# Performance work log

Hardware: AMD Instinct MI355X
Metric: run time of the kernel (lower is better)

## Reference

```python
import jax, jax.numpy as jnp
import numpy as np
from jax import lax

B, N, C, H = 16, 577, 1024, 16
D = C // H          # head_dim = 64
M = 24              # spatial side, M*M = N-1
CH = C // 4         # conv bottleneck channels = 256
EPS = 1e-5


def _ln(x, g, b):
    mu = jnp.mean(x, axis=-1, keepdims=True)
    var = jnp.mean((x - mu) ** 2, axis=-1, keepdims=True)
    return (x - mu) * lax.rsqrt(var + EPS) * g + b


def setup_inputs() -> dict:
    key = jax.random.key(0)
    ks = jax.random.split(key, 8)
    s = 0.02
    return {
        "x": jax.random.normal(ks[0], (B, N, C), jnp.float32),
        "ln1_g": jnp.ones((C,), jnp.float32),
        "ln1_b": jnp.zeros((C,), jnp.float32),
        "in_w": jax.random.normal(ks[1], (3 * C, C), jnp.float32) * s,
        "in_b": jnp.zeros((3 * C,), jnp.float32),
        "out_w": jax.random.normal(ks[2], (C, C), jnp.float32) * s,
        "out_b": jnp.zeros((C,), jnp.float32),
        "ln2_g": jnp.ones((C,), jnp.float32),
        "ln2_b": jnp.zeros((C,), jnp.float32),
        "conv1_w": jax.random.normal(ks[3], (CH, C, 3, 3), jnp.float32) * s,
        "conv1_b": jnp.zeros((CH,), jnp.float32),
        "conv2_w": jax.random.normal(ks[4], (C, CH, 3, 3), jnp.float32) * s,
        "conv2_b": jnp.zeros((C,), jnp.float32),
    }


def reference(x, ln1_g, ln1_b, in_w, in_b, out_w, out_b, ln2_g, ln2_b,
              conv1_w, conv1_b, conv2_w, conv2_b):
    residual = x
    h = _ln(x, ln1_g, ln1_b)
    # qkv projection: (B,N,3C) -> (3,B,H,N,D)
    qkv = (h @ in_w.T + in_b).reshape(B, N, 3, H, D).transpose(2, 0, 3, 1, 4)
    q, k, v = qkv[0], qkv[1], qkv[2]
    scale = D ** (-0.5)
    scores = jnp.einsum("bhnd,bhmd->bhnm", q, k) * scale   # (B,H,N,N)
    attn = jax.nn.softmax(scores, axis=-1)
    o = jnp.einsum("bhnm,bhmd->bhnd", attn, v)
    o = o.transpose(0, 2, 1, 3).reshape(B, N, C)
    o = o @ out_w.T + out_b
    x = o + residual                                       # first residual

    y = _ln(x, ln2_g, ln2_b)
    f = y[:, :-1, :].reshape(B, M, M, C).transpose(0, 3, 1, 2)   # NCHW
    c = y[:, -1:, :]                                             # class token
    f = lax.conv_general_dilated(f, conv1_w, (1, 1), "SAME",
                                 dimension_numbers=("NCHW", "OIHW", "NCHW"))
    f = jax.nn.gelu(f + conv1_b[None, :, None, None])
    f = lax.conv_general_dilated(f, conv2_w, (1, 1), "SAME",
                                 dimension_numbers=("NCHW", "OIHW", "NCHW"))
    f = f + conv2_b[None, :, None, None]
    f = f.transpose(0, 2, 3, 1).reshape(B, N - 1, C)
    y = jnp.concatenate((f, c), axis=1)
    return x + y
```

## Files before the change

### kernel.cpp

```cpp
#include <hip/hip_runtime.h>

typedef unsigned short u16;
typedef unsigned int u32;
typedef __bf16 bf16x8 __attribute__((ext_vector_type(8)));
typedef float f32x4 __attribute__((ext_vector_type(4)));

#define DEVI __device__ __forceinline__

#define BB 16
#define NN 577
#define CC 1024
#define HH 16
#define DD 64
#define BN 9232
#define PIX 576
#define WW 24
#define CHN 256
#define VROW 584
#define PSZ (9216 * 256)

DEVI u16 f2b(float f) {
  u32 u = __builtin_bit_cast(u32, f);
  u32 r = 0x7FFFu + ((u >> 16) & 1u);
  return (u16)((u + r) >> 16);
}

DEVI float b2f(u16 h) { return __builtin_bit_cast(float, (u32)h << 16); }

DEVI bf16x8 ldfrag(const u16* p) {
  uint4 u = *(const uint4*)p;
  return __builtin_bit_cast(bf16x8, u);
}

DEVI f32x4 mfma16(bf16x8 a, bf16x8 b, f32x4 c) {
  return __builtin_amdgcn_mfma_f32_16x16x32_bf16(a, b, c, 0, 0, 0);
}

DEVI void gld_lds16(const u16* g, u16* l) {
  __builtin_amdgcn_global_load_lds((const __attribute__((address_space(1))) void*)g,
                                   (__attribute__((address_space(3))) void*)l, 16, 0, 0);
}

DEVI float gelu_tanh(float v) {
  const float x3 = v * v * v;
  const float t = __expf(1.5957691216057308f * (v + 0.044715f * x3));
  const float th = (t - 1.f) / (t + 1.f);
  return 0.5f * v * (1.f + th);
}

__global__ __launch_bounds__(256) void prep_kernel(
    const float* __restrict__ in_w, const float* __restrict__ out_w,
    const float* __restrict__ c1w, const float* __restrict__ c2w,
    u16* __restrict__ wqkv, u16* __restrict__ wout,
    u16* __restrict__ w1t, u16* __restrict__ w2t, u16* __restrict__ zpad) {
  const int i0 = blockIdx.x * 256 + threadIdx.x;
  const int stride = gridDim.x * 256;
  for (int i = i0; i < 3072 * 1024; i += stride) wqkv[i] = f2b(in_w[i]);
  for (int i = i0; i < 1024 * 1024; i += stride) wout[i] = f2b(out_w[i]);
  for (int i = i0; i < 256 * 9216; i += stride) {
    int oc = i / 9216, rem = i - oc * 9216, tap = rem >> 10, c = rem & 1023;
    w1t[i] = f2b(c1w[(size_t)oc * 9216 + c * 9 + tap]);
  }
  for (int i = i0; i < 1024 * 2304; i += stride) {
    int oc = i / 2304, rem = i - oc * 2304, tap = rem >> 8, c = rem & 255;
    w2t[i] = f2b(c2w[(size_t)oc * 2304 + c * 9 + tap]);
  }
  if (i0 < 128) zpad[i0] = 0;
}

template <int MODE>
__global__ __launch_bounds__(256) void ln_kernel(
    const float* __restrict__ xin, const float* __restrict__ gam,
    const float* __restrict__ bet, u16* __restrict__ yout, float* __restrict__ oextra) {
  __shared__ float sh[8];
  const int row = blockIdx.x;
  const int tid = threadIdx.x;
  const float4 v = ((const float4*)(xin + (size_t)row * CC))[tid];
  float s = v.x + v.y + v.z + v.w;
  float qq = v.x * v.x + v.y * v.y + v.z * v.z + v.w * v.w;
#pragma unroll
  for (int off = 32; off > 0; off >>= 1) {
    s += __shfl_down(s, off);
    qq += __shfl_down(qq, off);
  }
  if ((tid & 63) == 0) { sh[tid >> 6] = s; sh[4 + (tid >> 6)] = qq; }
  __syncthreads();
  s = sh[0] + sh[1] + sh[2] + sh[3];
  qq = sh[4] + sh[5] + sh[6] + sh[7];
  const float mu = s * (1.f / 1024.f);
  const float rstd = rsqrtf(qq * (1.f / 1024.f) - mu * mu + 1e-5f);
  const float4 g4 = ((const float4*)gam)[tid];
  const float4 b4 = ((const float4*)bet)[tid];
  const float o0 = (v.x - mu) * rstd * g4.x + b4.x;
  const float o1 = (v.y - mu) * rstd * g4.y + b4.y;
  const float o2 = (v.z - mu) * rstd * g4.z + b4.z;
  const float o3 = (v.w - mu) * rstd * g4.w + b4.w;
  ushort4 st = make_ushort4(f2b(o0), f2b(o1), f2b(o2), f2b(o3));
  *(ushort4*)(yout + (size_t)row * CC + tid * 4) = st;
  if constexpr (MODE == 1) {
    if (row % NN == NN - 1) {
      float4 ov = make_float4(v.x + o0, v.y + o1, v.z + o2, v.w + o3);
      ((float4*)(oextra + (size_t)row * CC))[tid] = ov;
    }
  }
}

struct GArgs {
  const u16* A; const u16* Bm; const float* bias; const float* res;
  float* outF; u16* outH; u16* outQ; u16* outK; u16* outV; const u16* zpad;
  int M, K;
};

template <int MODE>
__global__ __launch_bounds__(256) void gemm_kernel(GArgs ag) {
  __shared__ u16 SH[24576];
  const int tid = threadIdx.x;
  const int w = tid >> 6, l = tid & 63;
  const int wr = w >> 1, wc = w & 1;
  const int lr = l & 15, lg = l >> 4;
  const int m0 = blockIdx.x * 128, n0 = blockIdx.y * 128;
  const int tapz = (MODE == 4) ? blockIdx.z : 0;
  const int rA = w * 16 + (l >> 2);
  const int cbs = ((l & 3) ^ ((l >> 3) & 3)) * 8;

  auto stage = [&](int buf, int kt) {
    const int k0 = kt * 32;
    u16* Ald = SH + buf * 4096;
    u16* Bld = SH + 12288 + buf * 4096;
#pragma unroll
    for (int c = 0; c < 2; ++c) {
      const int r = c * 64 + rA;
      const u16* asrc;
      if constexpr (MODE <= 1) {
        int m = m0 + r;
        m = m < ag.M ? m : ag.M - 1;
        asrc = ag.A + (size_t)m * ag.K + (k0 + cbs);
      } else {
        const int m = m0 + r;
        const int b = m / PIX, p = m - b * PIX;
        const int py = p / WW, px = p - py * WW;
        constexpr int CKc = (MODE == 3) ? 256 : 1024;
        const int tap = (MODE == 4) ? tapz : (k0 / CKc);
        const int c0 = (MODE == 4) ? k0 : (k0 - tap * CKc);
        const int py2 = py + (tap / 3) - 1, px2 = px + (tap % 3) - 1;
        if ((u32)py2 < (u32)WW && (u32)px2 < (u32)WW) {
          if constexpr (MODE == 4)
            asrc = ag.A + ((size_t)(b * NN + py2 * WW + px2) * CC + c0 + cbs);
          else
            asrc = ag.A + ((size_t)(b * PIX + py2 * WW + px2) * CHN + c0 + cbs);
        } else {
          asrc = ag.zpad + cbs;
        }
      }
      gld_lds16(asrc, &Ald[c * 2048 + w * 512]);
      const u16* bsrc;
      if constexpr (MODE == 4)
        bsrc = ag.Bm + (size_t)(n0 + r) * 9216 + (tapz * 1024 + k0 + cbs);
      else
        bsrc = ag.Bm + (size_t)(n0 + r) * ag.K + (k0 + cbs);
      gld_lds16(bsrc, &Bld[c * 2048 + w * 512]);
    }
  };

  f32x4 acc[4][4] = {};
  const int KL = (MODE == 4) ? 1024 : ag.K;
  const int nst = KL >> 5;

  stage(0, 0);
  stage(1, 1);

  const int swz = (lr >> 1) & 3;
  int b0 = 0, b1 = 1, b2 = 2;
  for (int kt = 0; kt < nst; ++kt) {
    if (kt + 1 < nst) { asm volatile("s_waitcnt vmcnt(4)" ::: "memory"); }
    else              { asm volatile("s_waitcnt vmcnt(0)" ::: "memory"); }
    __builtin_amdgcn_s_barrier();
    if (kt + 2 < nst) stage(b2, kt + 2);
    bf16x8 af[4], bfr[4];
#pragma unroll
    for (int i = 0; i < 4; ++i)
      af[i] = ldfrag(&SH[b0 * 4096 + (wr * 64 + i * 16 + lr) * 32 + ((lg ^ swz) * 8)]);
#pragma unroll
    for (int i = 0; i < 4; ++i)
      bfr[i] = ldfrag(&SH[12288 + b0 * 4096 + (wc * 64 + i * 16 + lr) * 32 + ((lg ^ swz) * 8)]);
    __builtin_amdgcn_s_setprio(1);
#pragma unroll
    for (int mi = 0; mi < 4; ++mi)
#pragma unroll
      for (int ni = 0; ni < 4; ++ni) acc[mi][ni] = mfma16(af[mi], bfr[ni], acc[mi][ni]);
    __builtin_amdgcn_s_setprio(0);
    const int tmp = b0; b0 = b1; b1 = b2; b2 = tmp;
  }

  if constexpr (MODE == 0) {
    if (n0 >= 2048) {
      __syncthreads();
      const int G0 = m0 + wr * 64;
      const int b0q = G0 / NN;
      const bool ok = (G0 + 63 < ag.M) && (b0q == (G0 + 63) / NN);
      const int h = (n0 + wc * 64 - 2048) >> 6;
      u16* scr = SH + w * 5120;
      if (ok) {
#pragma unroll
        for (int mi = 0; mi < 4; ++mi) {
#pragma unroll
          for (int ni = 0; ni < 4; ++ni) {
            ushort4 st;
            const float bv = ag.bias[n0 + wc * 64 + ni * 16 + lr];
            st.x = f2b(acc[mi][ni][0] + bv);
            st.y = f2b(acc[mi][ni][1] + bv);
            st.z = f2b(acc[mi][ni][2] + bv);
            st.w = f2b(acc[mi][ni][3] + bv);
            *(ushort4*)(scr + (ni * 16 + lr) * 80 + mi * 16 + lg * 4) = st;
          }
        }
        asm volatile("s_waitcnt lgkmcnt(0)" ::: "memory");
        const int nb = G0 - b0q * NN;
        u16* vb = ag.outV + (size_t)((b0q * 16 + h) * 64) * VROW;
#pragma unroll
        for (int pass = 0; pass < 8; ++pass) {
          const int d_ = pass * 8 + (l >> 3);
          const int nn = (l & 7) * 8;
          uint4 vv = *(const uint4*)(scr + d_ * 80 + nn);
          u16* dst = vb + (size_t)d_ * VROW + nb + nn;
          if (!(nb & 1)) {
            ((u32*)dst)[0] = vv.x; ((u32*)dst)[1] = vv.y;
            ((u32*)dst)[2] = vv.z; ((u32*)dst)[3] = vv.w;
          } else {
            u16 tmp[8];
            *(uint4*)tmp = vv;
#pragma unroll
            for (int j = 0; j < 8; ++j) dst[j] = tmp[j];
          }
        }
      } else {
#pragma unroll
        for (int mi = 0; mi < 4; ++mi) {
#pragma unroll
          for (int r = 0; r < 4; ++r) {
            const int row = G0 + mi * 16 + lg * 4 + r;
            if (row >= ag.M) continue;
            const int b = row / NN, n = row - b * NN;
#pragma unroll
            for (int ni = 0; ni < 4; ++ni) {
              const int col = n0 + wc * 64 + ni * 16 + lr;
              const int d = col & 63;
              const float v = acc[mi][ni][r] + ag.bias[col];
              ag.outV[((size_t)((b * 16 + h) * 64 + d)) * VROW + n] = f2b(v);
            }
          }
        }
      }
      return;
    }
#pragma unroll
    for (int mi = 0; mi < 4; ++mi) {
#pragma unroll
      for (int r = 0; r < 4; ++r) {
        const int row = m0 + wr * 64 + mi * 16 + lg * 4 + r;
        if (row >= ag.M) continue;
        const int b = row / NN, n = row - b * NN;
#pragma unroll
        for (int ni = 0; ni < 4; ++ni) {
          const int col = n0 + wc * 64 + ni * 16 + lr;
          const int which = col >> 10, hd = col & 1023, h = hd >> 6, d = hd & 63;
          const float v = acc[mi][ni][r] + ag.bias[col];
          if (which == 0)
            ag.outQ[((size_t)(b * 16 + h) * NN + n) * DD + d] = f2b(v * 0.18033688011112042f);
          else
            ag.outK[((size_t)(b * 16 + h) * NN + n) * DD + d] = f2b(v);
        }
      }
    }
  } else {
#pragma unroll
    for (int mi = 0; mi < 4; ++mi) {
#pragma unroll
      for (int r = 0; r < 4; ++r) {
        const int row = m0 + wr * 64 + mi * 16 + lg * 4 + r;
        if (row >= ag.M) continue;
#pragma unroll
        for (int ni = 0; ni < 4; ++ni) {
          const int col = n0 + wc * 64 + ni * 16 + lr;
          if constexpr (MODE == 4) {
            u16* pb = (tapz < 5) ? ag.outH : ag.outQ;
            const int tl = (tapz < 5) ? tapz : tapz - 5;
            pb[(size_t)tl * PSZ + (size_t)row * CHN + col] = f2b(acc[mi][ni][r]);
          } else {
            const float v = acc[mi][ni][r] + ag.bias[col];
            if constexpr (MODE == 1) {
              const size_t idx = (size_t)row * CC + col;
              ag.outF[idx] = v + ag.res[idx];
            } else {
              const int b = row / PIX, p = row - b * PIX;
              const size_t idx = (size_t)(b * NN + p) * CC + col;
              ag.outF[idx] = v + ag.res[idx];
            }
          }
        }
      }
    }
  }
}

__global__ __launch_bounds__(256) void gelu_reduce_kernel(
    const u16* __restrict__ pA, const u16* __restrict__ pB,
    const float* __restrict__ bias, u16* __restrict__ f1) {
  const size_t i4 = ((size_t)blockIdx.x * 256 + threadIdx.x) * 4;
  const int col = (int)(i4 & 255);
  float s0 = 0.f, s1 = 0.f, s2 = 0.f, s3 = 0.f;
#pragma unroll
  for (int t = 0; t < 5; ++t) {
    ushort4 u = *(const ushort4*)(pA + (size_t)t * PSZ + i4);
    s0 += b2f(u.x); s1 += b2f(u.y); s2 += b2f(u.z); s3 += b2f(u.w);
  }
#pragma unroll
  for (int t = 0; t < 4; ++t) {
    ushort4 u = *(const ushort4*)(pB + (size_t)t * PSZ + i4);
    s0 += b2f(u.x); s1 += b2f(u.y); s2 += b2f(u.z); s3 += b2f(u.w);
  }
  const float4 b4 = *(const float4*)(bias + col);
  ushort4 st = make_ushort4(f2b(gelu_tanh(s0 + b4.x)), f2b(gelu_tanh(s1 + b4.y)),
                            f2b(gelu_tanh(s2 + b4.z)), f2b(gelu_tanh(s3 + b4.w)));
  *(ushort4*)(f1 + i4) = st;
}

__global__ __launch_bounds__(512) void attn_kernel(
    const u16* __restrict__ q, const u16* __restrict__ k,
    const u16* __restrict__ vt, u16* __restrict__ o) {
  __shared__ u16 SH2[24576];
  const int tid = threadIdx.x;
  const int w = tid >> 6, l = tid & 63;
  const int lr = l & 15, lg = l >> 4;
  const int lg4 = lg * 4;
  const int bid = blockIdx.x;
  const int xcd = bid & 7, gg = bid >> 3;
  const int bh = (gg / 5) * 8 + xcd;
  const int qt = gg % 5;
  const int b = bh >> 4, h = bh & 15;

  const u16* qp = q + (size_t)bh * NN * DD;
  const u16* kp = k + (size_t)bh * NN * DD;
  const u16* vp = vt + (size_t)bh * DD * VROW;

  const int qrow = qt * 128 + w * 16 + lr;
  const int qrc = qrow < NN ? qrow : NN - 1;
  const bf16x8 qf0 = ldfrag(qp + (size_t)qrc * DD + lg * 8);
  const bf16x8 qf1 = ldfrag(qp + (size_t)qrc * DD + 32 + lg * 8);

  const int srow = l >> 3;
  const int schk = (l & 7) ^ (srow & 7);
  auto stage = [&](int buf, int kt) {
    const int kb = kt * 64;
    gld_lds16(kp + (size_t)(kb + w * 8 + srow) * DD + schk * 8,
              &SH2[buf * 4096 + w * 512]);
    gld_lds16(vp + (size_t)(w * 8 + srow) * VROW + kb + schk * 8,
              &SH2[8192 + buf * 4096 + w * 512]);
  };

  f32x4 oa[4] = {};
  float mrow = -1e30f;
  float lsum = 0.f;
  u16* pw = &SH2[16384 + w * 1024];
  const int x7 = lr & 7;
  const int x3 = lr & 3;

  stage(0, 0);
  stage(1, 1);

  for (int kt = 0; kt < 10; ++kt) {
    if (kt <= 7) { asm volatile("s_waitcnt vmcnt(2)" ::: "memory"); }
    else         { asm volatile("s_waitcnt vmcnt(0)" ::: "memory"); }
    __builtin_amdgcn_s_barrier();
    const u16* KB = &SH2[(kt & 1) * 4096];
    const u16* VB = &SH2[8192 + (kt & 1) * 4096];
    const int kb = kt * 64;

    f32x4 s[4] = {};
#pragma unroll
    for (int g = 0; g < 4; ++g) {
      const int row = g * 16 + lr;
      const bf16x8 a0 = ldfrag(&KB[row * 64 + ((lg ^ x7) * 8)]);
      const bf16x8 a1 = ldfrag(&KB[row * 64 + (((4 + lg) ^ x7) * 8)]);
      s[g] = mfma16(a0, qf0, s[g]);
      s[g] = mfma16(a1, qf1, s[g]);
    }
    float t[16];
    const bool last = (kt == 9);
#pragma unroll
    for (int g = 0; g < 4; ++g)
#pragma unroll
      for (int r = 0; r < 4; ++r) {
        const int key = kb + g * 16 + lg4 + r;
        t[g * 4 + r] = (!last || key < NN) ? s[g][r] : -3e38f;
      }
    float pmax = t[0];
#pragma unroll
    for (int i = 1; i < 16; ++i) pmax = fmaxf(pmax, t[i]);
    pmax = fmaxf(pmax, __shfl_xor(pmax, 16));
    pmax = fmaxf(pmax, __shfl_xor(pmax, 32));
    if (!__all(pmax <= mrow + 8.f)) {
      const float mn = fmaxf(mrow, pmax);
      const float corr = exp2f(mrow - mn);
      mrow = mn;
      lsum *= corr;
      float bc[4];
#pragma unroll
      for (int r = 0; r < 4; ++r) bc[r] = __shfl(corr, (l & 48) | (lg4 + r));
#pragma unroll
      for (int g = 0; g < 4; ++g)
#pragma unroll
        for (int r = 0; r < 4; ++r) oa[g][r] *= bc[r];
    }
    float ps[16];
    float rsum = 0.f;
#pragma unroll
    for (int i = 0; i < 16; ++i) { ps[i] = exp2f(t[i] - mrow); rsum += ps[i]; }
    rsum += __shfl_xor(rsum, 16);
    rsum += __shfl_xor(rsum, 32);
    lsum += rsum;
#pragma unroll
    for (int g = 0; g < 4; ++g) {
      u32 w0, w1;
      asm("v_cvt_pk_bf16_f32 %0, %1, %2" : "=v"(w0) : "v"(ps[g * 4 + 0]), "v"(ps[g * 4 + 1]));
      asm("v_cvt_pk_bf16_f32 %0, %1, %2" : "=v"(w1) : "v"(ps[g * 4 + 2]), "v"(ps[g * 4 + 3]));
      const int lc = (g & 1) * 2 + (lg >> 1);
      const int off = (g >> 1) * 512 + lr * 32 + ((lc ^ x3) * 8) + (lg & 1) * 4;
      *(uint2*)(&pw[off]) = make_uint2(w0, w1);
    }
    asm volatile("s_waitcnt lgkmcnt(0)" ::: "memory");
    const bf16x8 paf = ldfrag(&pw[lr * 32 + ((lg ^ x3) * 8)]);
    const bf16x8 pbf = ldfrag(&pw[512 + lr * 32 + ((lg ^ x3) * 8)]);
#pragma unroll
    for (int dg = 0; dg < 4; ++dg) {
      const int row = dg * 16 + lr;
      const bf16x8 v0 = ldfrag(&VB[row * 64 + ((lg ^ x7) * 8)]);
      const bf16x8 v1 = ldfrag(&VB[row * 64 + (((4 + lg) ^ x7) * 8)]);
      oa[dg] = mfma16(paf, v0, oa[dg]);
      oa[dg] = mfma16(pbf, v1, oa[dg]);
    }
    asm volatile("s_waitcnt lgkmcnt(0)" ::: "memory");
    __builtin_amdgcn_s_barrier();
    if (kt + 2 <= 9) stage(kt & 1, kt + 2);
  }

  const int nq = qt * 128 + w * 16 + lg4;
  float linv[4];
#pragma unroll
  for (int r = 0; r < 4; ++r) linv[r] = __shfl(lsum, (l & 48) | (lg4 + r));
#pragma unroll
  for (int r = 0; r < 4; ++r) {
    const int n = nq + r;
    if (n >= NN) continue;
    const float inv = 1.0f / linv[r];
#pragma unroll
    for (int g = 0; g < 4; ++g)
      o[(size_t)(b * NN + n) * CC + h * DD + g * 16 + lr] = f2b(oa[g][r] * inv);
  }
}

extern "C" void kernel_launch(void* const* d_in, const int* in_sizes, int n_in,
                              void* d_out, int out_size, void* d_ws, size_t ws_size,
                              hipStream_t stream) {
  const float* x     = (const float*)d_in[0];
  const float* ln1_g = (const float*)d_in[1];
  const float* ln1_b = (const float*)d_in[2];
  const float* in_w  = (const float*)d_in[3];
  const float* in_b  = (const float*)d_in[4];
  const float* out_w = (const float*)d_in[5];
  const float* out_b = (const float*)d_in[6];
  const float* ln2_g = (const float*)d_in[7];
  const float* ln2_b = (const float*)d_in[8];
  const float* c1w   = (const float*)d_in[9];
  const float* c1b   = (const float*)d_in[10];
  const float* c2w   = (const float*)d_in[11];
  const float* c2b   = (const float*)d_in[12];
  float* out = (float*)d_out;

  char* ws = (char*)d_ws;
  size_t off = 0;
  auto alloc = [&](size_t bytes) {
    void* p = ws + off;
    off += (bytes + 255) & ~(size_t)255;
    return p;
  };
  u16* hb   = (u16*)alloc((size_t)BN * CC * 2);
  u16* wqkv = (u16*)alloc((size_t)3072 * 1024 * 2);
  u16* wout = (u16*)alloc((size_t)1024 * 1024 * 2);
  u16* w1t  = (u16*)alloc((size_t)256 * 9216 * 2);
  u16* w2t  = (u16*)alloc((size_t)1024 * 2304 * 2);
  u16* qb   = (u16*)alloc((size_t)256 * NN * DD * 2);
  u16* kb   = (u16*)alloc((size_t)256 * NN * DD * 2);
  u16* vtb  = (u16*)alloc((size_t)256 * DD * VROW * 2 + 16384);
  float* x2 = (float*)alloc((size_t)BN * CC * 4);
  u16* zpad = (u16*)alloc(256);
  u16* ob = hb;
  u16* yb = qb;
  u16* f1 = kb;
  u16* pA = hb;
  u16* pB = vtb;

  prep_kernel<<<1024, 256, 0, stream>>>(in_w, out_w, c1w, c2w, wqkv, wout, w1t, w2t, zpad);
  ln_kernel<0><<<BN, 256, 0, stream>>>(x, ln1_g, ln1_b, hb, nullptr);
  {
    GArgs a{hb, wqkv, in_b, nullptr, nullptr, nullptr, qb, kb, vtb, zpad, BN, CC};
    gemm_kernel<0><<<dim3(73, 24), 256, 0, stream>>>(a);
  }
  attn_kernel<<<1280, 512, 0, stream>>>(qb, kb, vtb, ob);
  {
    GArgs a{ob, wout, out_b, x, x2, nullptr, nullptr, nullptr, nullptr, zpad, BN, CC};
    gemm_kernel<1><<<dim3(73, 8), 256, 0, stream>>>(a);
  }
  ln_kernel<1><<<BN, 256, 0, stream>>>(x2, ln2_g, ln2_b, yb, out);
  {
    GArgs a{yb, w1t, c1b, nullptr, nullptr, pA, pB, nullptr, nullptr, zpad, 9216, 9216};
    gemm_kernel<4><<<dim3(72, 2, 9), 256, 0, stream>>>(a);
  }
  gelu_reduce_kernel<<<2304, 256, 0, stream>>>(pA, pB, c1b, f1);
  {
    GArgs a{f1, w2t, c2b, x2, out, nullptr, nullptr, nullptr, nullptr, zpad, 9216, 2304};
    gemm_kernel<3><<<dim3(72, 8), 256, 0, stream>>>(a);
  }
}
```

Before: 399.4 us.

## Enlarge GEMM tiles to 256x128, remap block order, store residual x2 in bf16

The GEMM kernel now computes 256x128 output tiles, with each wave holding 8x4 MFMA accumulators. It uses a 1-D grid with a custom block-to-tile mapping so that neighbouring blocks share weight or activation tiles, and it sets launch bounds to two blocks per CU. The intermediate residual x2 is stored as bf16 instead of fp32, halving that tensor's write and read traffic in the out-proj epilogue, LN2 and the conv2 epilogue. The larger tiles raise register and LDS use and may lower occupancy. The bf16 residual loses precision in the final sum.

```diff
diff --git a/kernel.cpp b/kernel.cpp
--- a/kernel.cpp
+++ b/kernel.cpp
@@ -70,12 +70,19 @@
 
 template <int MODE>
 __global__ __launch_bounds__(256) void ln_kernel(
-    const float* __restrict__ xin, const float* __restrict__ gam,
-    const float* __restrict__ bet, u16* __restrict__ yout, float* __restrict__ oextra) {
+    const float* __restrict__ xf, const u16* __restrict__ xh,
+    const float* __restrict__ gam, const float* __restrict__ bet,
+    u16* __restrict__ yout, float* __restrict__ oextra) {
   __shared__ float sh[8];
   const int row = blockIdx.x;
   const int tid = threadIdx.x;
-  const float4 v = ((const float4*)(xin + (size_t)row * CC))[tid];
+  float4 v;
+  if constexpr (MODE == 0) {
+    v = ((const float4*)(xf + (size_t)row * CC))[tid];
+  } else {
+    ushort4 uv = ((const ushort4*)(xh + (size_t)row * CC))[tid];
+    v = make_float4(b2f(uv.x), b2f(uv.y), b2f(uv.z), b2f(uv.w));
+  }
   float s = v.x + v.y + v.z + v.w;
   float qq = v.x * v.x + v.y * v.y + v.z * v.z + v.w * v.w;
 #pragma unroll
@@ -106,63 +113,77 @@
 }
 
 struct GArgs {
-  const u16* A; const u16* Bm; const float* bias; const float* res;
+  const u16* A; const u16* Bm; const float* bias; const float* res; const u16* resH;
   float* outF; u16* outH; u16* outQ; u16* outK; u16* outV; const u16* zpad;
   int M, K;
 };
 
 template <int MODE>
-__global__ __launch_bounds__(256) void gemm_kernel(GArgs ag) {
-  __shared__ u16 SH[24576];
+__global__ __launch_bounds__(256, 2) void gemm_kernel(GArgs ag) {
+  __shared__ u16 SH[36864];
   const int tid = threadIdx.x;
   const int w = tid >> 6, l = tid & 63;
-  const int wr = w >> 1, wc = w & 1;
+  const int wm = w >> 1, wn = w & 1;
   const int lr = l & 15, lg = l >> 4;
-  const int m0 = blockIdx.x * 128, n0 = blockIdx.y * 128;
-  const int tapz = (MODE == 4) ? blockIdx.z : 0;
-  const int rA = w * 16 + (l >> 2);
-  const int cbs = ((l & 3) ^ ((l >> 3) & 3)) * 8;
+  const int bid = blockIdx.x;
+  int mt, nt, tapz = 0;
+  if constexpr (MODE == 0) {
+    const int i = bid >> 3;
+    mt = i / 3; nt = (bid & 7) * 3 + (i - mt * 3);
+  } else if constexpr (MODE == 1 || MODE == 3) {
+    nt = bid & 7; mt = bid >> 3;
+  } else {
+    const int g = (bid & 7) * 81 + (bid >> 3);
+    tapz = g / 72;
+    const int rem = g - tapz * 72;
+    mt = rem >> 1; nt = rem & 1;
+  }
+  const int m0 = mt * 256, n0 = nt * 128;
+  const int rr = tid >> 2;
+  const int cbs = ((tid & 3) ^ ((tid >> 3) & 3)) * 8;
+
+  auto aSrc = [&](int r, int k0) -> const u16* {
+    if constexpr (MODE <= 1) {
+      int m = m0 + r;
+      m = m < ag.M ? m : ag.M - 1;
+      return ag.A + (size_t)m * ag.K + (k0 + cbs);
+    } else {
+      const int m = m0 + r;
+      const int b = m / PIX, p = m - b * PIX;
+      const int py = p / WW, px = p - py * WW;
+      constexpr int CKc = (MODE == 3) ? 256 : 1024;
+      const int tap = (MODE == 4) ? tapz : (k0 / CKc);
+      const int c0 = (MODE == 4) ? k0 : (k0 - tap * CKc);
+      const int py2 = py + (tap / 3) - 1, px2 = px + (tap % 3) - 1;
+      if ((u32)py2 < (u32)WW && (u32)px2 < (u32)WW) {
+        if constexpr (MODE == 4)
+          return ag.A + ((size_t)(b * NN + py2 * WW + px2) * CC + c0 + cbs);
+        else
+          return ag.A + ((size_t)(b * PIX + py2 * WW + px2) * CHN + c0 + cbs);
+      }
+      return ag.zpad + cbs;
+    }
+  };
 
   auto stage = [&](int buf, int kt) {
     const int k0 = kt * 32;
-    u16* Ald = SH + buf * 4096;
-    u16* Bld = SH + 12288 + buf * 4096;
-#pragma unroll
-    for (int c = 0; c < 2; ++c) {
-      const int r = c * 64 + rA;
-      const u16* asrc;
-      if constexpr (MODE <= 1) {
-        int m = m0 + r;
-        m = m < ag.M ? m : ag.M - 1;
-        asrc = ag.A + (size_t)m * ag.K + (k0 + cbs);
-      } else {
-        const int m = m0 + r;
-        const int b = m / PIX, p = m - b * PIX;
-        const int py = p / WW, px = p - py * WW;
-        constexpr int CKc = (MODE == 3) ? 256 : 1024;
-        const int tap = (MODE == 4) ? tapz : (k0 / CKc);
-        const int c0 = (MODE == 4) ? k0 : (k0 - tap * CKc);
-        const int py2 = py + (tap / 3) - 1, px2 = px + (tap % 3) - 1;
-        if ((u32)py2 < (u32)WW && (u32)px2 < (u32)WW) {
-          if constexpr (MODE == 4)
-            asrc = ag.A + ((size_t)(b * NN + py2 * WW + px2) * CC + c0 + cbs);
-          else
-            asrc = ag.A + ((size_t)(b * PIX + py2 * WW + px2) * CHN + c0 + cbs);
-        } else {
-          asrc = ag.zpad + cbs;
-        }
-      }
-      gld_lds16(asrc, &Ald[c * 2048 + w * 512]);
+    u16* Ald = SH + buf * 8192;
+    u16* Bld = SH + 24576 + buf * 4096;
+#pragma unroll
+    for (int j = 0; j < 4; ++j)
+      gld_lds16(aSrc(j * 64 + rr, k0), &Ald[j * 2048 + w * 512]);
+#pragma unroll
+    for (int j = 0; j < 2; ++j) {
       const u16* bsrc;
       if constexpr (MODE == 4)
-        bsrc = ag.Bm + (size_t)(n0 + r) * 9216 + (tapz * 1024 + k0 + cbs);
+        bsrc = ag.Bm + (size_t)(n0 + j * 64 + rr) * 9216 + (tapz * 1024 + k0 + cbs);
       else
-        bsrc = ag.Bm + (size_t)(n0 + r) * ag.K + (k0 + cbs);
-      gld_lds16(bsrc, &Bld[c * 2048 + w * 512]);
+        bsrc = ag.Bm + (size_t)(n0 + j * 64 + rr) * ag.K + (k0 + cbs);
+      gld_lds16(bsrc, &Bld[j * 2048 + w * 512]);
     }
   };
 
-  f32x4 acc[4][4] = {};
+  f32x4 acc[8][4] = {};
   const int KL = (MODE == 4) ? 1024 : ag.K;
   const int nst = KL >> 5;
 
@@ -172,20 +193,20 @@
   const int swz = (lr >> 1) & 3;
   int b0 = 0, b1 = 1, b2 = 2;
   for (int kt = 0; kt < nst; ++kt) {
-    if (kt + 1 < nst) { asm volatile("s_waitcnt vmcnt(4)" ::: "memory"); }
+    if (kt + 1 < nst) { asm volatile("s_waitcnt vmcnt(6)" ::: "memory"); }
     else              { asm volatile("s_waitcnt vmcnt(0)" ::: "memory"); }
     __builtin_amdgcn_s_barrier();
     if (kt + 2 < nst) stage(b2, kt + 2);
-    bf16x8 af[4], bfr[4];
+    bf16x8 af[8], bfr[4];
+#pragma unroll
+    for (int i = 0; i < 8; ++i)
+      af[i] = ldfrag(&SH[b0 * 8192 + (wm * 128 + i * 16 + lr) * 32 + ((lg ^ swz) * 8)]);
 #pragma unroll
     for (int i = 0; i < 4; ++i)
-      af[i] = ldfrag(&SH[b0 * 4096 + (wr * 64 + i * 16 + lr) * 32 + ((lg ^ swz) * 8)]);
-#pragma unroll
-    for (int i = 0; i < 4; ++i)
-      bfr[i] = ldfrag(&SH[12288 + b0 * 4096 + (wc * 64 + i * 16 + lr) * 32 + ((lg ^ swz) * 8)]);
+      bfr[i] = ldfrag(&SH[24576 + b0 * 4096 + (wn * 64 + i * 16 + lr) * 32 + ((lg ^ swz) * 8)]);
     __builtin_amdgcn_s_setprio(1);
 #pragma unroll
-    for (int mi = 0; mi < 4; ++mi)
+    for (int mi = 0; mi < 8; ++mi)
 #pragma unroll
       for (int ni = 0; ni < 4; ++ni) acc[mi][ni] = mfma16(af[mi], bfr[ni], acc[mi][ni]);
     __builtin_amdgcn_s_setprio(0);
@@ -195,58 +216,63 @@
   if constexpr (MODE == 0) {
     if (n0 >= 2048) {
       __syncthreads();
-      const int G0 = m0 + wr * 64;
-      const int b0q = G0 / NN;
-      const bool ok = (G0 + 63 < ag.M) && (b0q == (G0 + 63) / NN);
-      const int h = (n0 + wc * 64 - 2048) >> 6;
+      const int hh = (n0 + wn * 64 - 2048) >> 6;
       u16* scr = SH + w * 5120;
-      if (ok) {
-#pragma unroll
-        for (int mi = 0; mi < 4; ++mi) {
-#pragma unroll
-          for (int ni = 0; ni < 4; ++ni) {
-            ushort4 st;
-            const float bv = ag.bias[n0 + wc * 64 + ni * 16 + lr];
-            st.x = f2b(acc[mi][ni][0] + bv);
-            st.y = f2b(acc[mi][ni][1] + bv);
-            st.z = f2b(acc[mi][ni][2] + bv);
-            st.w = f2b(acc[mi][ni][3] + bv);
-            *(ushort4*)(scr + (ni * 16 + lr) * 80 + mi * 16 + lg * 4) = st;
+#pragma unroll
+      for (int qh = 0; qh < 2; ++qh) {
+        if (qh) { asm volatile("s_waitcnt lgkmcnt(0)" ::: "memory"); }
+        const int G0 = m0 + wm * 128 + qh * 64;
+        const int b0q = G0 / NN;
+        const bool ok = (G0 + 63 < ag.M) && (b0q == (G0 + 63) / NN);
+        if (ok) {
+#pragma unroll
+          for (int mi = 0; mi < 4; ++mi) {
+#pragma unroll
+            for (int ni = 0; ni < 4; ++ni) {
+              const f32x4 a4 = acc[qh * 4 + mi][ni];
+              const float bv = ag.bias[n0 + wn * 64 + ni * 16 + lr];
+              ushort4 st;
+              st.x = f2b(a4[0] + bv);
+              st.y = f2b(a4[1] + bv);
+              st.z = f2b(a4[2] + bv);
+              st.w = f2b(a4[3] + bv);
+              *(ushort4*)(scr + (ni * 16 + lr) * 80 + mi * 16 + lg * 4) = st;
+            }
           }
-        }
-        asm volatile("s_waitcnt lgkmcnt(0)" ::: "memory");
-        const int nb = G0 - b0q * NN;
-        u16* vb = ag.outV + (size_t)((b0q * 16 + h) * 64) * VROW;
-#pragma unroll
-        for (int pass = 0; pass < 8; ++pass) {
-          const int d_ = pass * 8 + (l >> 3);
-          const int nn = (l & 7) * 8;
-          uint4 vv = *(const uint4*)(scr + d_ * 80 + nn);
-          u16* dst = vb + (size_t)d_ * VROW + nb + nn;
-          if (!(nb & 1)) {
-            ((u32*)dst)[0] = vv.x; ((u32*)dst)[1] = vv.y;
-            ((u32*)dst)[2] = vv.z; ((u32*)dst)[3] = vv.w;
-          } else {
-            u16 tmp[8];
-            *(uint4*)tmp = vv;
-#pragma unroll
-            for (int j = 0; j < 8; ++j) dst[j] = tmp[j];
+          asm volatile("s_waitcnt lgkmcnt(0)" ::: "memory");
+          const int nb = G0 - b0q * NN;
+          u16* vb = ag.outV + (size_t)((b0q * 16 + hh) * 64) * VROW;
+#pragma unroll
+          for (int pass = 0; pass < 8; ++pass) {
+            const int d_ = pass * 8 + (l >> 3);
+            const int nn = (l & 7) * 8;
+            uint4 vv = *(const uint4*)(scr + d_ * 80 + nn);
+            u16* dst = vb + (size_t)d_ * VROW + nb + nn;
+            if (!(nb & 1)) {
+              ((u32*)dst)[0] = vv.x; ((u32*)dst)[1] = vv.y;
+              ((u32*)dst)[2] = vv.z; ((u32*)dst)[3] = vv.w;
+            } else {
+              u16 tmp[8];
+              *(uint4*)tmp = vv;
+#pragma unroll
+              for (int j = 0; j < 8; ++j) dst[j] = tmp[j];
+            }
           }
-        }
-      } else {
-#pragma unroll
-        for (int mi = 0; mi < 4; ++mi) {
-#pragma unroll
-          for (int r = 0; r < 4; ++r) {
-            const int row = G0 + mi * 16 + lg * 4 + r;
-            if (row >= ag.M) continue;
-            const int b = row / NN, n = row - b * NN;
-#pragma unroll
-            for (int ni = 0; ni < 4; ++ni) {
-              const int col = n0 + wc * 64 + ni * 16 + lr;
-              const int d = col & 63;
-              const float v = acc[mi][ni][r] + ag.bias[col];
-              ag.outV[((size_t)((b * 16 + h) * 64 + d)) * VROW + n] = f2b(v);
+        } else {
+#pragma unroll
+          for (int mi = 0; mi < 4; ++mi) {
+#pragma unroll
+            for (int r = 0; r < 4; ++r) {
+              const int row = G0 + mi * 16 + lg * 4 + r;
+              if (row >= ag.M) continue;
+              const int b = row / NN, n = row - b * NN;
+#pragma unroll
+              for (int ni = 0; ni < 4; ++ni) {
+                const int col = n0 + wn * 64 + ni * 16 + lr;
+                const int d = col & 63;
+                const float v = acc[qh * 4 + mi][ni][r] + ag.bias[col];
+                ag.outV[((size_t)((b * 16 + hh) * 64 + d)) * VROW + n] = f2b(v);
+              }
             }
           }
         }
@@ -254,15 +280,15 @@
       return;
     }
 #pragma unroll
-    for (int mi = 0; mi < 4; ++mi) {
+    for (int mi = 0; mi < 8; ++mi) {
 #pragma unroll
       for (int r = 0; r < 4; ++r) {
-        const int row = m0 + wr * 64 + mi * 16 + lg * 4 + r;
+        const int row = m0 + wm * 128 + mi * 16 + lg * 4 + r;
         if (row >= ag.M) continue;
         const int b = row / NN, n = row - b * NN;
 #pragma unroll
         for (int ni = 0; ni < 4; ++ni) {
-          const int col = n0 + wc * 64 + ni * 16 + lr;
+          const int col = n0 + wn * 64 + ni * 16 + lr;
           const int which = col >> 10, hd = col & 1023, h = hd >> 6, d = hd & 63;
           const float v = acc[mi][ni][r] + ag.bias[col];
           if (which == 0)
@@ -274,28 +300,25 @@
     }
   } else {
 #pragma unroll
-    for (int mi = 0; mi < 4; ++mi) {
+    for (int mi = 0; mi < 8; ++mi) {
 #pragma unroll
       for (int r = 0; r < 4; ++r) {
-        const int row = m0 + wr * 64 + mi * 16 + lg * 4 + r;
+        const int row = m0 + wm * 128 + mi * 16 + lg * 4 + r;
         if (row >= ag.M) continue;
 #pragma unroll
         for (int ni = 0; ni < 4; ++ni) {
-          const int col = n0 + wc * 64 + ni * 16 + lr;
+          const int col = n0 + wn * 64 + ni * 16 + lr;
           if constexpr (MODE == 4) {
             u16* pb = (tapz < 5) ? ag.outH : ag.outQ;
             const int tl = (tapz < 5) ? tapz : tapz - 5;
             pb[(size_t)tl * PSZ + (size_t)row * CHN + col] = f2b(acc[mi][ni][r]);
+          } else if constexpr (MODE == 1) {
+            const size_t idx = (size_t)row * CC + col;
+            ag.outH[idx] = f2b(acc[mi][ni][r] + ag.bias[col] + ag.res[idx]);
           } else {
-            const float v = acc[mi][ni][r] + ag.bias[col];
-            if constexpr (MODE == 1) {
-              const size_t idx = (size_t)row * CC + col;
-              ag.outF[idx] = v + ag.res[idx];
-            } else {
-              const int b = row / PIX, p = row - b * PIX;
-              const size_t idx = (size_t)(b * NN + p) * CC + col;
-              ag.outF[idx] = v + ag.res[idx];
-            }
+            const int b = row / PIX, p = row - b * PIX;
+            const size_t idx = (size_t)(b * NN + p) * CC + col;
+            ag.outF[idx] = acc[mi][ni][r] + ag.bias[col] + b2f(ag.resH[idx]);
           }
         }
       }
@@ -492,7 +515,7 @@
   u16* qb   = (u16*)alloc((size_t)256 * NN * DD * 2);
   u16* kb   = (u16*)alloc((size_t)256 * NN * DD * 2);
   u16* vtb  = (u16*)alloc((size_t)256 * DD * VROW * 2 + 16384);
-  float* x2 = (float*)alloc((size_t)BN * CC * 4);
+  u16* x2h  = (u16*)alloc((size_t)BN * CC * 2);
   u16* zpad = (u16*)alloc(256);
   u16* ob = hb;
   u16* yb = qb;
@@ -501,24 +524,24 @@
   u16* pB = vtb;
 
   prep_kernel<<<1024, 256, 0, stream>>>(in_w, out_w, c1w, c2w, wqkv, wout, w1t, w2t, zpad);
-  ln_kernel<0><<<BN, 256, 0, stream>>>(x, ln1_g, ln1_b, hb, nullptr);
+  ln_kernel<0><<<BN, 256, 0, stream>>>(x, nullptr, ln1_g, ln1_b, hb, nullptr);
   {
-    GArgs a{hb, wqkv, in_b, nullptr, nullptr, nullptr, qb, kb, vtb, zpad, BN, CC};
-    gemm_kernel<0><<<dim3(73, 24), 256, 0, stream>>>(a);
+    GArgs a{hb, wqkv, in_b, nullptr, nullptr, nullptr, nullptr, qb, kb, vtb, zpad, BN, CC};
+    gemm_kernel<0><<<888, 256, 0, stream>>>(a);
   }
   attn_kernel<<<1280, 512, 0, stream>>>(qb, kb, vtb, ob);
   {
-    GArgs a{ob, wout, out_b, x, x2, nullptr, nullptr, nullptr, nullptr, zpad, BN, CC};
-    gemm_kernel<1><<<dim3(73, 8), 256, 0, stream>>>(a);
-  }
-  ln_kernel<1><<<BN, 256, 0, stream>>>(x2, ln2_g, ln2_b, yb, out);
+    GArgs a{ob, wout, out_b, x, nullptr, nullptr, x2h, nullptr, nullptr, nullptr, zpad, BN, CC};
+    gemm_kernel<1><<<296, 256, 0, stream>>>(a);
+  }
+  ln_kernel<1><<<BN, 256, 0, stream>>>(nullptr, x2h, ln2_g, ln2_b, yb, out);
   {
-    GArgs a{yb, w1t, c1b, nullptr, nullptr, pA, pB, nullptr, nullptr, zpad, 9216, 9216};
-    gemm_kernel<4><<<dim3(72, 2, 9), 256, 0, stream>>>(a);
+    GArgs a{yb, w1t, c1b, nullptr, nullptr, nullptr, pA, pB, nullptr, nullptr, zpad, 9216, 9216};
+    gemm_kernel<4><<<648, 256, 0, stream>>>(a);
   }
   gelu_reduce_kernel<<<2304, 256, 0, stream>>>(pA, pB, c1b, f1);
   {
-    GArgs a{f1, w2t, c2b, x2, out, nullptr, nullptr, nullptr, nullptr, zpad, 9216, 2304};
-    gemm_kernel<3><<<dim3(72, 8), 256, 0, stream>>>(a);
-  }
-}
+    GArgs a{f1, w2t, c2b, nullptr, x2h, out, nullptr, nullptr, nullptr, nullptr, zpad, 9216, 2304};
+    gemm_kernel<3><<<288, 256, 0, stream>>>(a);
+  }
+}
```

Result: slower. 420.2 us (+5.2%).
